# Kernel optimization log

Measured on AMD Instinct MI355X. Metric: run time of the kernel, lower is better.

The kernel has to match this reference:

```python
import jax, jax.numpy as jnp
import numpy as np

B, S, D, H, HD, NU, T = 64, 512, 256, 4, 64, 100000, 24


def setup_inputs() -> dict:
    key = jax.random.key(0)
    ks = jax.random.split(key, 13)
    return {
        "timeslot_embedded": jax.random.normal(ks[0], (T, D), jnp.float32),
        "user": jax.random.randint(ks[1], (B,), 0, NU, dtype=jnp.int64) if jax.config.jax_enable_x64 else jax.random.randint(ks[1], (B,), 0, NU, dtype=jnp.int32),
        "hour": jax.random.randint(ks[2], (B, S), 0, T, dtype=jnp.int32),
        "hour_mask": jax.random.randint(ks[3], (B, S, T), 0, 2, dtype=jnp.int32),
        "user_pref": jax.random.normal(ks[4], (NU, D), jnp.float32) * 0.02,
        "Wq": jax.random.normal(ks[5], (H, HD, 2 * D), jnp.float32) * 0.02,
        "bq": jnp.zeros((H, HD), jnp.float32),
        "Wk": jax.random.normal(ks[6], (H, HD, D), jnp.float32) * 0.02,
        "bk": jnp.zeros((H, HD), jnp.float32),
        "Wv": jax.random.normal(ks[7], (H, HD, D), jnp.float32) * 0.02,
        "bv": jnp.zeros((H, HD), jnp.float32),
        "Wu": jax.random.normal(ks[8], (D, D), jnp.float32) * 0.02,
        "bu": jnp.zeros((D,), jnp.float32),
    }


def reference(timeslot_embedded, user, hour, hour_mask, user_pref,
              Wq, bq, Wk, bk, Wv, bv, Wu, bu):
    b, s = hour.shape
    n = b * s
    # per-token features
    user_feat = jnp.broadcast_to(user_pref[user][:, None, :], (b, s, D)).reshape(n, D)
    time_feat = timeslot_embedded[hour.reshape(n)]          # [N, D]
    query = jnp.concatenate([user_feat, time_feat], axis=-1)  # [N, 2D]
    # all heads at once (equivalent to the per-head Linear loop)
    q = jnp.einsum('nd,hkd->nhk', query, Wq) + bq[None]               # [N, H, HD]
    k = jnp.einsum('td,hkd->htk', timeslot_embedded, Wk) + bk[:, None, :]  # [H, T, HD]
    v = jnp.einsum('td,hkd->htk', timeslot_embedded, Wv) + bv[:, None, :]  # [H, T, HD]
    scale = 1.0 / np.sqrt(HD).astype(np.float32)
    scores = jnp.einsum('nhk,htk->nht', q, k) * scale                 # [N, H, T]
    mask = hour_mask.reshape(n, T)[:, None, :]                        # [N, 1, T]
    scores = jnp.where(mask == 1, -jnp.inf, scores)
    attn = jax.nn.softmax(scores, axis=-1)
    out = jnp.einsum('nht,htk->nhk', attn, v).reshape(n, H * HD)      # concat heads
    out = out @ Wu.T + bu
    return out.reshape(b, s, D)
```

## Files before the change

kernel.cpp:

```cpp
#include <hip/hip_runtime.h>
#include <hip/hip_bf16.h>

#define QU_OFF   0
#define QT_OFF   16384
#define KK_OFF   22528
#define VV_OFF   28672
#define EU_OFF   34816
#define ET_OFF   40960
#define VWB_OFF  43264

typedef __attribute__((ext_vector_type(8))) short bf16x8;
typedef __attribute__((ext_vector_type(4))) float f32x4;

__device__ __forceinline__ unsigned short f2bf(float f) {
    unsigned u = __builtin_bit_cast(unsigned, f);
    return (unsigned short)((u + 0x7FFFu + ((u >> 16) & 1u)) >> 16);
}

__global__ __launch_bounds__(256) void precompA(
    const float* __restrict__ ts, const int* __restrict__ user,
    const float* __restrict__ user_pref,
    const float* __restrict__ Wq, const float* __restrict__ bq,
    const float* __restrict__ Wk, const float* __restrict__ bk,
    const float* __restrict__ Wv, const float* __restrict__ bv,
    float* __restrict__ ws)
{
    int tid = threadIdx.x;
    int lane = tid & 63;
    int gw = blockIdx.x * 4 + (tid >> 6);
    const float* wrow; const float* x; float bias = 0.f; float* outp;
    if (gw < 16384) {
        int b = gw >> 8, j = gw & 255;
        wrow = Wq + j * 512;
        x = user_pref + (long long)user[b] * 256;
        outp = ws + QU_OFF + gw;
    } else if (gw < 22528) {
        int r = gw - 16384, t = r >> 8, j = r & 255;
        wrow = Wq + j * 512 + 256; x = ts + t * 256; bias = bq[j];
        outp = ws + QT_OFF + r;
    } else if (gw < 28672) {
        int r = gw - 22528, t = r >> 8, j = r & 255;
        wrow = Wk + j * 256; x = ts + t * 256; bias = bk[j];
        outp = ws + KK_OFF + ((j >> 6) * 24 + t) * 64 + (j & 63);
    } else {
        int r = gw - 28672, t = r >> 8, j = r & 255;
        wrow = Wv + j * 256; x = ts + t * 256; bias = bv[j];
        outp = ws + VV_OFF + ((j >> 6) * 24 + t) * 64 + (j & 63);
    }
    float s = 0.f;
    #pragma unroll
    for (int i = 0; i < 4; ++i) s = fmaf(wrow[lane + 64 * i], x[lane + 64 * i], s);
    #pragma unroll
    for (int off = 32; off; off >>= 1) s += __shfl_xor(s, off);
    if (lane == 0) *outp = s + bias;
}

__global__ __launch_bounds__(256) void precompB(float* __restrict__ ws,
                                                const float* __restrict__ Wu)
{
    const float* qu = ws + QU_OFF;
    const float* qt = ws + QT_OFF;
    const float* kk = ws + KK_OFF;
    const float* vv = ws + VV_OFF;
    int o = blockIdx.x * 256 + threadIdx.x;
    if (o < 12288) {
        int htp = o >> 8, d = o & 255;
        int ht = htp * 2;
        int h = ht / 24;
        const float4* v0 = (const float4*)(vv + ht * 64);
        const float4* v1 = (const float4*)(vv + ht * 64 + 64);
        const float4* wp = (const float4*)(Wu + d * 256 + h * 64);
        float s0 = 0.f, s1 = 0.f;
        #pragma unroll
        for (int i = 0; i < 16; ++i) {
            float4 wv = wp[i], a = v0[i], c = v1[i];
            s0 = fmaf(a.x, wv.x, fmaf(a.y, wv.y, fmaf(a.z, wv.z, fmaf(a.w, wv.w, s0))));
            s1 = fmaf(c.x, wv.x, fmaf(c.y, wv.y, fmaf(c.z, wv.z, fmaf(c.w, wv.w, s1))));
        }
        int kt = ht >> 5, nt = d >> 4, lg = (ht >> 3) & 3, jh = (ht & 7) >> 1;
        unsigned pack = (unsigned)f2bf(s0) | ((unsigned)f2bf(s1) << 16);
        ((unsigned*)(ws + VWB_OFF))[(kt * 16 + nt) * 256 + ((d & 15) + 16 * lg) * 4 + jh] = pack;
    } else if (o < 18432) {
        int o2 = o - 12288;
        int b = o2 / 96, rem = o2 - b * 96;
        const float* qp = qu + b * 256 + (rem / 24) * 64;
        const float* kp = kk + rem * 64;
        float s = 0.f;
        #pragma unroll 8
        for (int hd = 0; hd < 64; ++hd) s = fmaf(qp[hd], kp[hd], s);
        ws[EU_OFF + o2] = expf(s * 0.125f);
    } else if (o < 20736) {
        int o3 = o - 18432;
        int tp = o3 / 96, rem = o3 - tp * 96;
        const float* qp = qt + tp * 256 + (rem / 24) * 64;
        const float* kp = kk + rem * 64;
        float s = 0.f;
        #pragma unroll 8
        for (int hd = 0; hd < 64; ++hd) s = fmaf(qp[hd], kp[hd], s);
        ws[ET_OFF + o3] = expf(s * 0.125f);
    }
}

__global__ __launch_bounds__(256) void attn_mfma(
    const int* __restrict__ hour, const int* __restrict__ hour_mask,
    const float* __restrict__ ws, const float* __restrict__ bu,
    float* __restrict__ out)
{
    const float* EU = ws + EU_OFF;
    const float* ET = ws + ET_OFF;
    __shared__ int4 A_lds[12 * 64];
    int tid = threadIdx.x;
    int nb = blockIdx.x * 64;
    int b = nb >> 9;
    {
        int tok = tid >> 2, h = tid & 3;
        int n = nb + tok;
        int th = hour[n];
        const float4* EUp = (const float4*)(EU + b * 96 + h * 24);
        const float4* ETp = (const float4*)(ET + th * 96 + h * 24);
        const int4*   mp  = (const int4*)(hour_mask + (long long)n * 24);
        float p[24]; float ssum = 0.f;
        #pragma unroll
        for (int q = 0; q < 6; ++q) {
            float4 e = EUp[q]; float4 f = ETp[q]; int4 m = mp[q];
            float v0 = (m.x != 0) ? 0.f : e.x * f.x;
            float v1 = (m.y != 0) ? 0.f : e.y * f.y;
            float v2 = (m.z != 0) ? 0.f : e.z * f.z;
            float v3 = (m.w != 0) ? 0.f : e.w * f.w;
            p[q*4+0] = v0; p[q*4+1] = v1; p[q*4+2] = v2; p[q*4+3] = v3;
            ssum += (v0 + v1) + (v2 + v3);
        }
        float r = 1.0f / ssum;
        int mt = tok >> 4, tl = tok & 15;
        #pragma unroll
        for (int tp = 0; tp < 12; ++tp) {
            int ht = h * 24 + tp * 2;
            unsigned pack = (unsigned)f2bf(p[tp*2] * r)
                          | ((unsigned)f2bf(p[tp*2+1] * r) << 16);
            int kt = ht >> 5, lg = (ht >> 3) & 3, jh = (ht & 7) >> 1;
            ((unsigned*)A_lds)[((kt * 4 + mt) * 64 + tl + 16 * lg) * 4 + jh] = pack;
        }
    }
    __syncthreads();
    int w = tid >> 6, l = tid & 63;
    const int4* Bg = (const int4*)(ws + VWB_OFF);
    bf16x8 afr[3][4], bfr[3][4];
    #pragma unroll
    for (int kt = 0; kt < 3; ++kt)
        #pragma unroll
        for (int q = 0; q < 4; ++q) {
            afr[kt][q] = __builtin_bit_cast(bf16x8, A_lds[(kt * 4 + q) * 64 + l]);
            bfr[kt][q] = __builtin_bit_cast(bf16x8, Bg[(kt * 16 + w * 4 + q) * 64 + l]);
        }
    f32x4 acc[4][4];
    #pragma unroll
    for (int mt = 0; mt < 4; ++mt)
        #pragma unroll
        for (int q = 0; q < 4; ++q) acc[mt][q] = (f32x4)0.f;
    #pragma unroll
    for (int kt = 0; kt < 3; ++kt)
        #pragma unroll
        for (int mt = 0; mt < 4; ++mt)
            #pragma unroll
            for (int q = 0; q < 4; ++q)
                acc[mt][q] = __builtin_amdgcn_mfma_f32_16x16x32_bf16(
                    afr[kt][mt], bfr[kt][q], acc[mt][q], 0, 0, 0);
    int colb = w * 64 + (l & 15);
    float buv[4];
    #pragma unroll
    for (int q = 0; q < 4; ++q) buv[q] = bu[colb + q * 16];
    int row0 = nb + (l >> 4) * 4;
    #pragma unroll
    for (int mt = 0; mt < 4; ++mt)
        #pragma unroll
        for (int q = 0; q < 4; ++q) {
            float* op = out + (size_t)(row0 + mt * 16) * 256 + colb + q * 16;
            #pragma unroll
            for (int r = 0; r < 4; ++r)
                op[(size_t)r * 256] = acc[mt][q][r] + buv[q];
        }
}

extern "C" void kernel_launch(void* const* d_in, const int* in_sizes, int n_in,
                              void* d_out, int out_size, void* d_ws, size_t ws_size,
                              hipStream_t stream)
{
    const float* ts        = (const float*)d_in[0];
    const int*   user      = (const int*)  d_in[1];
    const int*   hour      = (const int*)  d_in[2];
    const int*   hour_mask = (const int*)  d_in[3];
    const float* user_pref = (const float*)d_in[4];
    const float* Wq        = (const float*)d_in[5];
    const float* bq        = (const float*)d_in[6];
    const float* Wk        = (const float*)d_in[7];
    const float* bk        = (const float*)d_in[8];
    const float* Wv        = (const float*)d_in[9];
    const float* bv        = (const float*)d_in[10];
    const float* Wu        = (const float*)d_in[11];
    const float* bu        = (const float*)d_in[12];
    float* ws  = (float*)d_ws;
    float* out = (float*)d_out;

    hipLaunchKernelGGL(precompA, dim3(8704), dim3(256), 0, stream,
                       ts, user, user_pref, Wq, bq, Wk, bk, Wv, bv, ws);
    hipLaunchKernelGGL(precompB, dim3(81), dim3(256), 0, stream, ws, Wu);
    hipLaunchKernelGGL(attn_mfma, dim3(512), dim3(256), 0, stream,
                       hour, hour_mask, ws, bu, out);
}
```

Baseline: 26.12 us.

## Restructure precompute as per-row-block GEMV and stage B tile in LDS

The first precompute kernel switches from one wave per output element (8704 blocks with shuffle reductions) to one block per input row, staging the input vector in shared memory while each thread computes one output column with float4 loads. The q·k exp precompute is vectorised with float4 loads. The attention kernel now processes 128 tokens per 512-thread block and loads the shared bf16 V·Wu B operand into LDS once per block instead of each wave reading it from global, which halves block count. In the new GEMV, each thread reads a different weight row with strided float4 accesses, so global loads are poorly coalesced. The larger attention block also changes occupancy.

```diff
diff --git a/kernel.cpp b/kernel.cpp
--- a/kernel.cpp
+++ b/kernel.cpp
@@ -17,7 +17,7 @@
     return (unsigned short)((u + 0x7FFFu + ((u >> 16) & 1u)) >> 16);
 }
 
-__global__ __launch_bounds__(256) void precompA(
+__global__ __launch_bounds__(256) void precomp1(
     const float* __restrict__ ts, const int* __restrict__ user,
     const float* __restrict__ user_pref,
     const float* __restrict__ Wq, const float* __restrict__ bq,
@@ -25,37 +25,43 @@
     const float* __restrict__ Wv, const float* __restrict__ bv,
     float* __restrict__ ws)
 {
-    int tid = threadIdx.x;
-    int lane = tid & 63;
-    int gw = blockIdx.x * 4 + (tid >> 6);
-    const float* wrow; const float* x; float bias = 0.f; float* outp;
-    if (gw < 16384) {
-        int b = gw >> 8, j = gw & 255;
-        wrow = Wq + j * 512;
-        x = user_pref + (long long)user[b] * 256;
-        outp = ws + QU_OFF + gw;
-    } else if (gw < 22528) {
-        int r = gw - 16384, t = r >> 8, j = r & 255;
-        wrow = Wq + j * 512 + 256; x = ts + t * 256; bias = bq[j];
-        outp = ws + QT_OFF + r;
-    } else if (gw < 28672) {
-        int r = gw - 22528, t = r >> 8, j = r & 255;
-        wrow = Wk + j * 256; x = ts + t * 256; bias = bk[j];
-        outp = ws + KK_OFF + ((j >> 6) * 24 + t) * 64 + (j & 63);
+    __shared__ float xs[256];
+    int tid = threadIdx.x, blk = blockIdx.x;
+    int lane = tid & 63, jb = tid >> 6;
+    int j = tid;
+    const float* W; const float* xsrc;
+    int ldw, coff; float bval; float* outp;
+    if (blk < 64) {
+        xsrc = user_pref + (size_t)user[blk] * 256;
+        W = Wq; ldw = 512; coff = 0; bval = 0.f;
+        outp = ws + QU_OFF + blk * 256 + j;
+    } else if (blk < 88) {
+        int t = blk - 64;
+        xsrc = ts + t * 256; W = Wq; ldw = 512; coff = 256; bval = bq[j];
+        outp = ws + QT_OFF + t * 256 + j;
+    } else if (blk < 112) {
+        int t = blk - 88;
+        xsrc = ts + t * 256; W = Wk; ldw = 256; coff = 0; bval = bk[j];
+        outp = ws + KK_OFF + (jb * 24 + t) * 64 + lane;
     } else {
-        int r = gw - 28672, t = r >> 8, j = r & 255;
-        wrow = Wv + j * 256; x = ts + t * 256; bias = bv[j];
-        outp = ws + VV_OFF + ((j >> 6) * 24 + t) * 64 + (j & 63);
-    }
+        int t = blk - 112;
+        xsrc = ts + t * 256; W = Wv; ldw = 256; coff = 0; bval = bv[j];
+        outp = ws + VV_OFF + (jb * 24 + t) * 64 + lane;
+    }
+    xs[tid] = xsrc[tid];
+    __syncthreads();
+    const float4* wr  = (const float4*)(W + (size_t)j * ldw + coff);
+    const float4* xv4 = (const float4*)xs;
     float s = 0.f;
-    #pragma unroll
-    for (int i = 0; i < 4; ++i) s = fmaf(wrow[lane + 64 * i], x[lane + 64 * i], s);
-    #pragma unroll
-    for (int off = 32; off; off >>= 1) s += __shfl_xor(s, off);
-    if (lane == 0) *outp = s + bias;
-}
-
-__global__ __launch_bounds__(256) void precompB(float* __restrict__ ws,
+    #pragma unroll 16
+    for (int k = 0; k < 64; ++k) {
+        float4 w4 = wr[k]; float4 x4 = xv4[k];
+        s = fmaf(w4.x, x4.x, fmaf(w4.y, x4.y, fmaf(w4.z, x4.z, fmaf(w4.w, x4.w, s))));
+    }
+    *outp = s + bval;
+}
+
+__global__ __launch_bounds__(256) void precomp2(float* __restrict__ ws,
                                                 const float* __restrict__ Wu)
 {
     const float* qu = ws + QU_OFF;
@@ -83,35 +89,46 @@
     } else if (o < 18432) {
         int o2 = o - 12288;
         int b = o2 / 96, rem = o2 - b * 96;
-        const float* qp = qu + b * 256 + (rem / 24) * 64;
-        const float* kp = kk + rem * 64;
+        const float4* qp = (const float4*)(qu + b * 256 + (rem / 24) * 64);
+        const float4* kp = (const float4*)(kk + rem * 64);
         float s = 0.f;
-        #pragma unroll 8
-        for (int hd = 0; hd < 64; ++hd) s = fmaf(qp[hd], kp[hd], s);
+        #pragma unroll
+        for (int i = 0; i < 16; ++i) {
+            float4 a = qp[i], c = kp[i];
+            s = fmaf(a.x, c.x, fmaf(a.y, c.y, fmaf(a.z, c.z, fmaf(a.w, c.w, s))));
+        }
         ws[EU_OFF + o2] = expf(s * 0.125f);
     } else if (o < 20736) {
         int o3 = o - 18432;
         int tp = o3 / 96, rem = o3 - tp * 96;
-        const float* qp = qt + tp * 256 + (rem / 24) * 64;
-        const float* kp = kk + rem * 64;
+        const float4* qp = (const float4*)(qt + tp * 256 + (rem / 24) * 64);
+        const float4* kp = (const float4*)(kk + rem * 64);
         float s = 0.f;
-        #pragma unroll 8
-        for (int hd = 0; hd < 64; ++hd) s = fmaf(qp[hd], kp[hd], s);
+        #pragma unroll
+        for (int i = 0; i < 16; ++i) {
+            float4 a = qp[i], c = kp[i];
+            s = fmaf(a.x, c.x, fmaf(a.y, c.y, fmaf(a.z, c.z, fmaf(a.w, c.w, s))));
+        }
         ws[ET_OFF + o3] = expf(s * 0.125f);
     }
 }
 
-__global__ __launch_bounds__(256) void attn_mfma(
+__global__ __launch_bounds__(512) void attn_mfma(
     const int* __restrict__ hour, const int* __restrict__ hour_mask,
     const float* __restrict__ ws, const float* __restrict__ bu,
     float* __restrict__ out)
 {
     const float* EU = ws + EU_OFF;
     const float* ET = ws + ET_OFF;
-    __shared__ int4 A_lds[12 * 64];
-    int tid = threadIdx.x;
-    int nb = blockIdx.x * 64;
+    __shared__ int4 B_lds[48 * 64];
+    __shared__ int4 A_lds[24 * 64];
+    int tid = threadIdx.x, w = tid >> 6, l = tid & 63;
+    int nb = blockIdx.x * 128;
     int b = nb >> 9;
+    const int4* Bg = (const int4*)(ws + VWB_OFF);
+    int4 breg[6];
+    #pragma unroll
+    for (int i = 0; i < 6; ++i) breg[i] = Bg[(w * 6 + i) * 64 + l];
     {
         int tok = tid >> 2, h = tid & 3;
         int n = nb + tok;
@@ -131,26 +148,27 @@
             ssum += (v0 + v1) + (v2 + v3);
         }
         float r = 1.0f / ssum;
-        int mt = tok >> 4, tl = tok & 15;
+        int mt8 = tok >> 4, tl = tok & 15;
         #pragma unroll
         for (int tp = 0; tp < 12; ++tp) {
             int ht = h * 24 + tp * 2;
             unsigned pack = (unsigned)f2bf(p[tp*2] * r)
                           | ((unsigned)f2bf(p[tp*2+1] * r) << 16);
             int kt = ht >> 5, lg = (ht >> 3) & 3, jh = (ht & 7) >> 1;
-            ((unsigned*)A_lds)[((kt * 4 + mt) * 64 + tl + 16 * lg) * 4 + jh] = pack;
-        }
-    }
+            ((unsigned*)A_lds)[((kt * 8 + mt8) * 64 + tl + 16 * lg) * 4 + jh] = pack;
+        }
+    }
+    #pragma unroll
+    for (int i = 0; i < 6; ++i) B_lds[(w * 6 + i) * 64 + l] = breg[i];
     __syncthreads();
-    int w = tid >> 6, l = tid & 63;
-    const int4* Bg = (const int4*)(ws + VWB_OFF);
+    int mh = w >> 2, ns = w & 3;
     bf16x8 afr[3][4], bfr[3][4];
     #pragma unroll
     for (int kt = 0; kt < 3; ++kt)
         #pragma unroll
         for (int q = 0; q < 4; ++q) {
-            afr[kt][q] = __builtin_bit_cast(bf16x8, A_lds[(kt * 4 + q) * 64 + l]);
-            bfr[kt][q] = __builtin_bit_cast(bf16x8, Bg[(kt * 16 + w * 4 + q) * 64 + l]);
+            afr[kt][q] = __builtin_bit_cast(bf16x8, A_lds[(kt * 8 + mh * 4 + q) * 64 + l]);
+            bfr[kt][q] = __builtin_bit_cast(bf16x8, B_lds[(kt * 16 + ns * 4 + q) * 64 + l]);
         }
     f32x4 acc[4][4];
     #pragma unroll
@@ -165,11 +183,11 @@
             for (int q = 0; q < 4; ++q)
                 acc[mt][q] = __builtin_amdgcn_mfma_f32_16x16x32_bf16(
                     afr[kt][mt], bfr[kt][q], acc[mt][q], 0, 0, 0);
-    int colb = w * 64 + (l & 15);
+    int colb = ns * 64 + (l & 15);
     float buv[4];
     #pragma unroll
     for (int q = 0; q < 4; ++q) buv[q] = bu[colb + q * 16];
-    int row0 = nb + (l >> 4) * 4;
+    int row0 = nb + mh * 64 + (l >> 4) * 4;
     #pragma unroll
     for (int mt = 0; mt < 4; ++mt)
         #pragma unroll
@@ -201,9 +219,9 @@
     float* ws  = (float*)d_ws;
     float* out = (float*)d_out;
 
-    hipLaunchKernelGGL(precompA, dim3(8704), dim3(256), 0, stream,
+    hipLaunchKernelGGL(precomp1, dim3(136), dim3(256), 0, stream,
                        ts, user, user_pref, Wq, bq, Wk, bk, Wv, bv, ws);
-    hipLaunchKernelGGL(precompB, dim3(81), dim3(256), 0, stream, ws, Wu);
-    hipLaunchKernelGGL(attn_mfma, dim3(512), dim3(256), 0, stream,
+    hipLaunchKernelGGL(precomp2, dim3(81), dim3(256), 0, stream, ws, Wu);
+    hipLaunchKernelGGL(attn_mfma, dim3(256), dim3(512), 0, stream,
                        hour, hour_mask, ws, bu, out);
 }
```

New measurement: 30.00 us. +14.9%, slower.
